# Optimization experiments

Measured on AMD Instinct MI355X. Metric: run time of the kernel, lower is better.

Reference implementation:

```python
import jax, jax.numpy as jnp
import numpy as np

D_MODEL = 1024
D_FF = 4096
NUM_EXPERTS = 8
NUM_SLOTS = 2
LN_EPS = 1e-5


def setup_inputs() -> dict:
    key = jax.random.key(0)
    ks = jax.random.split(key, 4)
    x = jax.random.normal(ks[0], (4, 4096, D_MODEL), dtype=jnp.float32)
    slot_embeds = jax.random.normal(ks[1], (NUM_EXPERTS * NUM_SLOTS, D_MODEL), dtype=jnp.float32) * 0.02
    # per-expert MLP weights, stacked over expert axis (Linear bias=False)
    W1 = jax.random.normal(ks[2], (NUM_EXPERTS, D_MODEL, D_FF), dtype=jnp.float32) * (1.0 / np.sqrt(D_MODEL))
    W2 = jax.random.normal(ks[3], (NUM_EXPERTS, D_FF, D_MODEL), dtype=jnp.float32) * (1.0 / np.sqrt(D_FF))
    ln_gamma = jnp.ones((D_MODEL,), dtype=jnp.float32)
    ln_beta = jnp.zeros((D_MODEL,), dtype=jnp.float32)
    return {"x": x, "slot_embeds": slot_embeds, "W1": W1, "W2": W2,
            "ln_gamma": ln_gamma, "ln_beta": ln_beta}


def reference(x, slot_embeds, W1, W2, ln_gamma, ln_beta):
    B, T, D = x.shape
    E, S = NUM_EXPERTS, NUM_SLOTS
    # logits: [B, T, E*S]
    logits = jnp.einsum('btd,nd->btn', x, slot_embeds) / jnp.sqrt(jnp.asarray(D, x.dtype))
    # dispatch: softmax over tokens (dim=1)
    dispatch = jax.nn.softmax(logits, axis=1)
    slot_in = jnp.einsum('btn,btd->bnd', dispatch, x)  # [B, E*S, D]
    # LayerNorm over last dim
    mu = jnp.mean(slot_in, axis=-1, keepdims=True)
    var = jnp.mean(jnp.square(slot_in - mu), axis=-1, keepdims=True)
    h = (slot_in - mu) * jax.lax.rsqrt(var + LN_EPS) * ln_gamma + ln_beta
    # per-expert MLP as a single batched (grouped) GEMM pair
    h = h.reshape(B, E, S, D)
    u = jax.nn.gelu(jnp.einsum('besd,edf->besf', h, W1), approximate=False)
    slot_out = jnp.einsum('besf,efd->besd', u, W2).reshape(B, E * S, D)
    # combine: softmax over slots (dim=2)
    combine = jax.nn.softmax(logits, axis=2)
    return jnp.einsum('btn,bnd->btd', combine, slot_out)
```

## Files before the change

kernel.cpp:

```cpp
#include <hip/hip_runtime.h>
#include <math.h>

#define NB 4
#define NT 4096
#define ND 1024
#define NS 16
#define NE 8
#define NF 4096

typedef float f32x4 __attribute__((ext_vector_type(4)));

__device__ __forceinline__ float gelu(float v) {
  return 0.5f * v * (1.f + erff(v * 0.70710678118654752f));
}
__device__ __forceinline__ void fma4(float4& a, float s, const float4& v) {
  a.x += s * v.x; a.y += s * v.y; a.z += s * v.z; a.w += s * v.w;
}
__device__ __forceinline__ float4 ld4(const float* p) {
  return *reinterpret_cast<const float4*>(p);
}
__device__ __forceinline__ float4 ld4nt(const float* p) {
  f32x4 v = __builtin_nontemporal_load(reinterpret_cast<const f32x4*>(p));
  return make_float4(v[0], v[1], v[2], v[3]);
}

__global__ __launch_bounds__(256, 4) void k_logits(const float* __restrict__ x,
                                                   const float* __restrict__ se,
                                                   float* __restrict__ logits) {
  const int wave = threadIdx.x >> 6, lane = threadIdx.x & 63;
  const int t0 = blockIdx.x * 16 + wave * 4;
  float acc[64];
#pragma unroll
  for (int j = 0; j < 64; ++j) acc[j] = 0.f;
  for (int it = 0; it < 4; ++it) {
    const int d = it * 256 + lane * 4;
    float4 xv[4];
#pragma unroll
    for (int tt = 0; tt < 4; ++tt)
      xv[tt] = ld4(x + (size_t)(t0 + tt) * ND + d);
#pragma unroll
    for (int n = 0; n < NS; ++n) {
      const float4 sv = ld4(se + (size_t)n * ND + d);
#pragma unroll
      for (int tt = 0; tt < 4; ++tt) {
        acc[tt * 16 + n] += xv[tt].x * sv.x + xv[tt].y * sv.y +
                            xv[tt].z * sv.z + xv[tt].w * sv.w;
      }
    }
  }
#pragma unroll
  for (int k = 0; k < 6; ++k) {
    const int dlt = 1 << k;
    const bool hi = (lane & dlt) != 0;
#pragma unroll
    for (int i = 0; i < (64 >> (k + 1)); ++i) {
      const float a = acc[2 * i], b = acc[2 * i + 1];
      const float send = hi ? a : b;
      const float recv = __shfl_xor(send, dlt, 64);
      acc[i] = (hi ? b : a) + recv;
    }
  }
  logits[(size_t)t0 * NS + lane] = acc[0] * 0.03125f;
}

__global__ __launch_bounds__(256) void k_softmax_stats(const float* __restrict__ logits,
                                                       float* __restrict__ stats) {
  int bn = blockIdx.x;
  int b = bn >> 4, n = bn & 15;
  __shared__ float red[256];
  const float* lp = logits + ((size_t)b * NT) * NS + n;
  float m = -1e30f;
  for (int t = threadIdx.x; t < NT; t += 256) m = fmaxf(m, lp[(size_t)t * NS]);
  red[threadIdx.x] = m; __syncthreads();
  for (int s = 128; s > 0; s >>= 1) {
    if (threadIdx.x < s) red[threadIdx.x] = fmaxf(red[threadIdx.x], red[threadIdx.x + s]);
    __syncthreads();
  }
  m = red[0]; __syncthreads();
  float sm = 0.f;
  for (int t = threadIdx.x; t < NT; t += 256) sm += expf(lp[(size_t)t * NS] - m);
  red[threadIdx.x] = sm; __syncthreads();
  for (int s = 128; s > 0; s >>= 1) {
    if (threadIdx.x < s) red[threadIdx.x] += red[threadIdx.x + s];
    __syncthreads();
  }
  if (threadIdx.x == 0) { stats[bn * 2] = m; stats[bn * 2 + 1] = red[0]; }
}

__global__ __launch_bounds__(256) void k_slot_in(const float* __restrict__ x,
                                                 const float* __restrict__ logits,
                                                 const float* __restrict__ stats,
                                                 float* __restrict__ si_part) {
  __shared__ float s_w[NS][64];
  const int tc = blockIdx.x, b = blockIdx.y;
  const int t0 = tc * 64;
  for (int i = threadIdx.x; i < NS * 64; i += 256) {
    const int n = i >> 6, t = i & 63;
    const float m = stats[(b * NS + n) * 2], s1 = stats[(b * NS + n) * 2 + 1];
    s_w[n][t] = expf(logits[((size_t)b * NT + t0 + t) * NS + n] - m) / s1;
  }
  __syncthreads();
  float4 acc[NS];
#pragma unroll
  for (int n = 0; n < NS; ++n) acc[n] = make_float4(0.f, 0.f, 0.f, 0.f);
  const int d = threadIdx.x * 4;
  const float* xb = x + ((size_t)b * NT + t0) * ND + d;
  float4 xv[2][8];
#pragma unroll
  for (int k = 0; k < 8; ++k) xv[0][k] = ld4(xb + (size_t)k * ND);
#pragma unroll
  for (int g = 0; g < 8; ++g) {
    const int cur = g & 1;
    if (g < 7) {
#pragma unroll
      for (int k = 0; k < 8; ++k)
        xv[cur ^ 1][k] = ld4(xb + (size_t)((g + 1) * 8 + k) * ND);
    }
#pragma unroll
    for (int n = 0; n < NS; ++n) {
      const float4 w0 = ld4(&s_w[n][g * 8]);
      const float4 w1 = ld4(&s_w[n][g * 8 + 4]);
      fma4(acc[n], w0.x, xv[cur][0]); fma4(acc[n], w0.y, xv[cur][1]);
      fma4(acc[n], w0.z, xv[cur][2]); fma4(acc[n], w0.w, xv[cur][3]);
      fma4(acc[n], w1.x, xv[cur][4]); fma4(acc[n], w1.y, xv[cur][5]);
      fma4(acc[n], w1.z, xv[cur][6]); fma4(acc[n], w1.w, xv[cur][7]);
    }
  }
#pragma unroll
  for (int n = 0; n < NS; ++n)
    *reinterpret_cast<float4*>(si_part + (((size_t)tc * 4 + b) * NS + n) * ND + d) = acc[n];
}

__global__ __launch_bounds__(256) void k_reduce_si(const float* __restrict__ si_part,
                                                   float* __restrict__ slot_in) {
  const int i = blockIdx.x * 256 + threadIdx.x;
  const int row = i >> 10, d = i & 1023;
  const int b = row >> 4, n = row & 15;
  float sum = 0.f;
  for (int tc = 0; tc < 64; ++tc)
    sum += si_part[(((size_t)tc * 4 + b) * NS + n) * ND + d];
  slot_in[i] = sum;
}

__global__ __launch_bounds__(256) void k_layernorm(float* __restrict__ slot_in,
                                                   const float* __restrict__ gamma,
                                                   const float* __restrict__ beta) {
  int row = blockIdx.x;
  __shared__ float red[256];
  float* rp = slot_in + (size_t)row * ND;
  float v[4];
  float sum = 0.f;
#pragma unroll
  for (int j = 0; j < 4; ++j) { v[j] = rp[threadIdx.x + j * 256]; sum += v[j]; }
  red[threadIdx.x] = sum; __syncthreads();
  for (int s = 128; s > 0; s >>= 1) {
    if (threadIdx.x < s) red[threadIdx.x] += red[threadIdx.x + s];
    __syncthreads();
  }
  float mu = red[0] * (1.f / ND); __syncthreads();
  float vs = 0.f;
#pragma unroll
  for (int j = 0; j < 4; ++j) { float t = v[j] - mu; vs += t * t; }
  red[threadIdx.x] = vs; __syncthreads();
  for (int s = 128; s > 0; s >>= 1) {
    if (threadIdx.x < s) red[threadIdx.x] += red[threadIdx.x + s];
    __syncthreads();
  }
  float rstd = rsqrtf(red[0] * (1.f / ND) + 1e-5f);
#pragma unroll
  for (int j = 0; j < 4; ++j) {
    int dd = threadIdx.x + j * 256;
    rp[dd] = (v[j] - mu) * rstd * gamma[dd] + beta[dd];
  }
}

__global__ __launch_bounds__(256) void k_mlp1(const float* __restrict__ h,
                                              const float* __restrict__ W1,
                                              float* __restrict__ u_part) {
  __shared__ float s_h[64][8];
  const int ft = blockIdx.x, dc = blockIdx.y, e = blockIdx.z;
  for (int i = threadIdx.x; i < 512; i += 256) {
    const int dd = i >> 3, j = i & 7;
    const int b = j >> 1, s = j & 1;
    s_h[dd][j] = h[((size_t)b * NS + e * 2 + s) * ND + dc * 64 + dd];
  }
  __syncthreads();
  float4 acc[8];
#pragma unroll
  for (int j = 0; j < 8; ++j) acc[j] = make_float4(0.f, 0.f, 0.f, 0.f);
  const int f = ft * 1024 + threadIdx.x * 4;
  const float* wb = W1 + ((size_t)e * ND + dc * 64) * NF + f;
  float4 wv[2][8];
#pragma unroll
  for (int k = 0; k < 8; ++k) wv[0][k] = ld4nt(wb + (size_t)k * NF);
#pragma unroll
  for (int g = 0; g < 8; ++g) {
    const int cur = g & 1;
    if (g < 7) {
#pragma unroll
      for (int k = 0; k < 8; ++k)
        wv[cur ^ 1][k] = ld4nt(wb + (size_t)((g + 1) * 8 + k) * NF);
    }
#pragma unroll
    for (int k = 0; k < 8; ++k) {
      const int dd = g * 8 + k;
      const float4 h0 = ld4(&s_h[dd][0]);
      const float4 h1 = ld4(&s_h[dd][4]);
      fma4(acc[0], h0.x, wv[cur][k]); fma4(acc[1], h0.y, wv[cur][k]);
      fma4(acc[2], h0.z, wv[cur][k]); fma4(acc[3], h0.w, wv[cur][k]);
      fma4(acc[4], h1.x, wv[cur][k]); fma4(acc[5], h1.y, wv[cur][k]);
      fma4(acc[6], h1.z, wv[cur][k]); fma4(acc[7], h1.w, wv[cur][k]);
    }
  }
#pragma unroll
  for (int j = 0; j < 8; ++j) {
    const int b = j >> 1, s = j & 1;
    const size_t row = ((size_t)b * NE + e) * 2 + s;
    *reinterpret_cast<float4*>(u_part + ((size_t)dc * 64 + row) * NF + f) = acc[j];
  }
}

__global__ __launch_bounds__(256) void k_mlp2(const float* __restrict__ u_part,
                                              const float* __restrict__ W2,
                                              float* __restrict__ so_part) {
  __shared__ float s_u[64][8];
  const int fc = blockIdx.x, e = blockIdx.y;
  for (int i = threadIdx.x; i < 512; i += 256) {
    const int j = i >> 6, ff = i & 63;
    const int b = j >> 1, s = j & 1;
    const size_t urow = ((size_t)b * NE + e) * 2 + s;
    float sum = 0.f;
    for (int dcc = 0; dcc < 16; ++dcc)
      sum += u_part[((size_t)dcc * 64 + urow) * NF + fc * 64 + ff];
    s_u[ff][j] = gelu(sum);
  }
  __syncthreads();
  float4 acc[8];
#pragma unroll
  for (int j = 0; j < 8; ++j) acc[j] = make_float4(0.f, 0.f, 0.f, 0.f);
  const int d = threadIdx.x * 4;
  const float* wb = W2 + ((size_t)e * NF + fc * 64) * ND + d;
  float4 wv[2][8];
#pragma unroll
  for (int k = 0; k < 8; ++k) wv[0][k] = ld4nt(wb + (size_t)k * ND);
#pragma unroll
  for (int g = 0; g < 8; ++g) {
    const int cur = g & 1;
    if (g < 7) {
#pragma unroll
      for (int k = 0; k < 8; ++k)
        wv[cur ^ 1][k] = ld4nt(wb + (size_t)((g + 1) * 8 + k) * ND);
    }
#pragma unroll
    for (int k = 0; k < 8; ++k) {
      const int ff = g * 8 + k;
      const float4 u0 = ld4(&s_u[ff][0]);
      const float4 u1 = ld4(&s_u[ff][4]);
      fma4(acc[0], u0.x, wv[cur][k]); fma4(acc[1], u0.y, wv[cur][k]);
      fma4(acc[2], u0.z, wv[cur][k]); fma4(acc[3], u0.w, wv[cur][k]);
      fma4(acc[4], u1.x, wv[cur][k]); fma4(acc[5], u1.y, wv[cur][k]);
      fma4(acc[6], u1.z, wv[cur][k]); fma4(acc[7], u1.w, wv[cur][k]);
    }
  }
#pragma unroll
  for (int j = 0; j < 8; ++j) {
    const int b = j >> 1, s = j & 1;
    const size_t row = (size_t)b * NS + e * 2 + s;
    *reinterpret_cast<float4*>(so_part + ((size_t)fc * 64 + row) * ND + d) = acc[j];
  }
}

__global__ __launch_bounds__(256) void k_reduce_so(const float* __restrict__ so_part,
                                                   float* __restrict__ slot_out) {
  const int i = blockIdx.x * 256 + threadIdx.x;
  float sum = 0.f;
  for (int fc = 0; fc < 64; ++fc)
    sum += so_part[(size_t)fc * 65536 + i];
  slot_out[i] = sum;
}

__global__ __launch_bounds__(256) void k_combine(const float* __restrict__ logits,
                                                 const float* __restrict__ slot_out,
                                                 float* __restrict__ out) {
  __shared__ float s_so[NS * ND];
  const int tb = blockIdx.x, b = blockIdx.y;
  for (int i = threadIdx.x; i < NS * ND; i += 256)
    s_so[i] = slot_out[(size_t)b * NS * ND + i];
  __syncthreads();
  const int wave = threadIdx.x >> 6, lane = threadIdx.x & 63;
  const int tbase = tb * 64 + wave * 16;
  for (int g = 0; g < 4; ++g) {
    const int t0 = tbase + g * 4;
    float c[4][NS];
#pragma unroll
    for (int tt = 0; tt < 4; ++tt) {
      const float* lp = logits + ((size_t)b * NT + t0 + tt) * NS;
      float l[NS];
      float m = -1e30f;
#pragma unroll
      for (int n = 0; n < NS; ++n) { l[n] = lp[n]; m = fmaxf(m, l[n]); }
      float s = 0.f;
#pragma unroll
      for (int n = 0; n < NS; ++n) { l[n] = expf(l[n] - m); s += l[n]; }
      const float rs = 1.f / s;
#pragma unroll
      for (int n = 0; n < NS; ++n) c[tt][n] = l[n] * rs;
    }
#pragma unroll
    for (int it = 0; it < 4; ++it) {
      const int d = it * 256 + lane * 4;
      float4 acc[4];
#pragma unroll
      for (int tt = 0; tt < 4; ++tt) acc[tt] = make_float4(0.f, 0.f, 0.f, 0.f);
#pragma unroll
      for (int n = 0; n < NS; ++n) {
        const float4 sv = ld4(&s_so[n * ND + d]);
        fma4(acc[0], c[0][n], sv); fma4(acc[1], c[1][n], sv);
        fma4(acc[2], c[2][n], sv); fma4(acc[3], c[3][n], sv);
      }
#pragma unroll
      for (int tt = 0; tt < 4; ++tt)
        *reinterpret_cast<float4*>(out + ((size_t)b * NT + t0 + tt) * ND + d) = acc[tt];
    }
  }
}

extern "C" void kernel_launch(void* const* d_in, const int* in_sizes, int n_in,
                              void* d_out, int out_size, void* d_ws, size_t ws_size,
                              hipStream_t stream) {
  const float* x     = (const float*)d_in[0];
  const float* se    = (const float*)d_in[1];
  const float* W1    = (const float*)d_in[2];
  const float* W2    = (const float*)d_in[3];
  const float* gamma = (const float*)d_in[4];
  const float* beta  = (const float*)d_in[5];
  float* out = (float*)d_out;

  float* ws       = (float*)d_ws;
  float* logits   = ws;
  float* stats    = ws + 262144;
  float* slot_in  = ws + 262400;
  float* slot_out = ws + 327936;
  float* si_part  = ws + 393472;
  float* u_part   = ws + 4587776;
  float* so_part  = ws + 8782080;

  k_logits<<<1024, 256, 0, stream>>>(x, se, logits);
  k_softmax_stats<<<NB * NS, 256, 0, stream>>>(logits, stats);
  k_slot_in<<<dim3(64, NB), 256, 0, stream>>>(x, logits, stats, si_part);
  k_reduce_si<<<256, 256, 0, stream>>>(si_part, slot_in);
  k_layernorm<<<NB * NS, 256, 0, stream>>>(slot_in, gamma, beta);
  k_mlp1<<<dim3(4, 16, NE), 256, 0, stream>>>(slot_in, W1, u_part);
  k_mlp2<<<dim3(64, NE), 256, 0, stream>>>(u_part, W2, so_part);
  k_reduce_so<<<256, 256, 0, stream>>>(so_part, slot_out);
  k_combine<<<dim3(64, NB), 256, 0, stream>>>(logits, slot_out, out);
}
```

Before: 448.2 us.

## Stream x and expert weights into LDS via async global_load_lds double buffering

In the slot_in, mlp1 and mlp2 kernels, register-held prefetches of x, W1 and W2 tiles are replaced with direct global-to-LDS loads (`__builtin_amdgcn_global_load_lds`, 16 bytes per lane) into a two-stage shared-memory ring. Each thread then reads its float4 from LDS, and a barrier ends each stage. The aim is to free vector registers and overlap streaming of the large weight and activation tiles with the FMA work. In exchange, each block now reserves 64KB of extra LDS, which lowers occupancy. It also adds a barrier per stage and drops the nontemporal load hint on the weight streams.

Result: slower. 462.5 us (+3.2%).

```diff
diff --git a/kernel.cpp b/kernel.cpp
--- a/kernel.cpp
+++ b/kernel.cpp
@@ -8,8 +8,6 @@
 #define NE 8
 #define NF 4096
 
-typedef float f32x4 __attribute__((ext_vector_type(4)));
-
 __device__ __forceinline__ float gelu(float v) {
   return 0.5f * v * (1.f + erff(v * 0.70710678118654752f));
 }
@@ -19,9 +17,10 @@
 __device__ __forceinline__ float4 ld4(const float* p) {
   return *reinterpret_cast<const float4*>(p);
 }
-__device__ __forceinline__ float4 ld4nt(const float* p) {
-  f32x4 v = __builtin_nontemporal_load(reinterpret_cast<const f32x4*>(p));
-  return make_float4(v[0], v[1], v[2], v[3]);
+__device__ __forceinline__ void gload_lds16(const float* gsrc, float* ldst) {
+  __builtin_amdgcn_global_load_lds(
+      (const __attribute__((address_space(1))) unsigned int*)gsrc,
+      (__attribute__((address_space(3))) unsigned int*)ldst, 16, 0, 0);
 }
 
 __global__ __launch_bounds__(256, 4) void k_logits(const float* __restrict__ x,
@@ -92,8 +91,16 @@
                                                  const float* __restrict__ stats,
                                                  float* __restrict__ si_part) {
   __shared__ float s_w[NS][64];
+  __shared__ float s_x[2][8 * 1024];
   const int tc = blockIdx.x, b = blockIdx.y;
   const int t0 = tc * 64;
+  const int wv = threadIdx.x >> 6, ln = threadIdx.x & 63;
+  const float* xb0 = x + ((size_t)b * NT + t0) * ND;
+#pragma unroll
+  for (int q = 0; q < 8; ++q) {
+    const int c = wv * 8 + q;
+    gload_lds16(xb0 + c * 256 + ln * 4, &s_x[0][c * 256]);
+  }
   for (int i = threadIdx.x; i < NS * 64; i += 256) {
     const int n = i >> 6, t = i & 63;
     const float m = stats[(b * NS + n) * 2], s1 = stats[(b * NS + n) * 2 + 1];
@@ -103,32 +110,33 @@
   float4 acc[NS];
 #pragma unroll
   for (int n = 0; n < NS; ++n) acc[n] = make_float4(0.f, 0.f, 0.f, 0.f);
-  const int d = threadIdx.x * 4;
-  const float* xb = x + ((size_t)b * NT + t0) * ND + d;
-  float4 xv[2][8];
-#pragma unroll
-  for (int k = 0; k < 8; ++k) xv[0][k] = ld4(xb + (size_t)k * ND);
-#pragma unroll
+  const int d4 = threadIdx.x * 4;
   for (int g = 0; g < 8; ++g) {
-    const int cur = g & 1;
     if (g < 7) {
-#pragma unroll
-      for (int k = 0; k < 8; ++k)
-        xv[cur ^ 1][k] = ld4(xb + (size_t)((g + 1) * 8 + k) * ND);
-    }
+      const float* src = xb0 + (size_t)(g + 1) * 8 * ND;
+#pragma unroll
+      for (int q = 0; q < 8; ++q) {
+        const int c = wv * 8 + q;
+        gload_lds16(src + c * 256 + ln * 4, &s_x[(g + 1) & 1][c * 256]);
+      }
+    }
+    const float* xt = &s_x[g & 1][0];
+    float4 xv[8];
+#pragma unroll
+    for (int k = 0; k < 8; ++k) xv[k] = ld4(xt + k * 1024 + d4);
 #pragma unroll
     for (int n = 0; n < NS; ++n) {
-      const float4 w0 = ld4(&s_w[n][g * 8]);
-      const float4 w1 = ld4(&s_w[n][g * 8 + 4]);
-      fma4(acc[n], w0.x, xv[cur][0]); fma4(acc[n], w0.y, xv[cur][1]);
-      fma4(acc[n], w0.z, xv[cur][2]); fma4(acc[n], w0.w, xv[cur][3]);
-      fma4(acc[n], w1.x, xv[cur][4]); fma4(acc[n], w1.y, xv[cur][5]);
-      fma4(acc[n], w1.z, xv[cur][6]); fma4(acc[n], w1.w, xv[cur][7]);
-    }
+      const float* wn = &s_w[n][g * 8];
+      fma4(acc[n], wn[0], xv[0]); fma4(acc[n], wn[1], xv[1]);
+      fma4(acc[n], wn[2], xv[2]); fma4(acc[n], wn[3], xv[3]);
+      fma4(acc[n], wn[4], xv[4]); fma4(acc[n], wn[5], xv[5]);
+      fma4(acc[n], wn[6], xv[6]); fma4(acc[n], wn[7], xv[7]);
+    }
+    __syncthreads();
   }
 #pragma unroll
   for (int n = 0; n < NS; ++n)
-    *reinterpret_cast<float4*>(si_part + (((size_t)tc * 4 + b) * NS + n) * ND + d) = acc[n];
+    *reinterpret_cast<float4*>(si_part + (((size_t)tc * 4 + b) * NS + n) * ND + d4) = acc[n];
 }
 
 __global__ __launch_bounds__(256) void k_reduce_si(const float* __restrict__ si_part,
@@ -178,7 +186,16 @@
                                               const float* __restrict__ W1,
                                               float* __restrict__ u_part) {
   __shared__ float s_h[64][8];
+  __shared__ float s_w1[2][8 * 1024];
   const int ft = blockIdx.x, dc = blockIdx.y, e = blockIdx.z;
+  const int wv = threadIdx.x >> 6, ln = threadIdx.x & 63;
+  const float* wb = W1 + ((size_t)e * ND + dc * 64) * NF + ft * 1024;
+#pragma unroll
+  for (int q = 0; q < 8; ++q) {
+    const int c = wv * 8 + q;
+    gload_lds16(wb + (size_t)(c >> 2) * NF + (c & 3) * 256 + ln * 4,
+                &s_w1[0][c * 1024 / 4]);
+  }
   for (int i = threadIdx.x; i < 512; i += 256) {
     const int dd = i >> 3, j = i & 7;
     const int b = j >> 1, s = j & 1;
@@ -188,30 +205,32 @@
   float4 acc[8];
 #pragma unroll
   for (int j = 0; j < 8; ++j) acc[j] = make_float4(0.f, 0.f, 0.f, 0.f);
-  const int f = ft * 1024 + threadIdx.x * 4;
-  const float* wb = W1 + ((size_t)e * ND + dc * 64) * NF + f;
-  float4 wv[2][8];
-#pragma unroll
-  for (int k = 0; k < 8; ++k) wv[0][k] = ld4nt(wb + (size_t)k * NF);
-#pragma unroll
+  const int f4 = threadIdx.x * 4;
   for (int g = 0; g < 8; ++g) {
-    const int cur = g & 1;
     if (g < 7) {
-#pragma unroll
-      for (int k = 0; k < 8; ++k)
-        wv[cur ^ 1][k] = ld4nt(wb + (size_t)((g + 1) * 8 + k) * NF);
-    }
+      const float* src = wb + (size_t)(g + 1) * 8 * NF;
+#pragma unroll
+      for (int q = 0; q < 8; ++q) {
+        const int c = wv * 8 + q;
+        gload_lds16(src + (size_t)(c >> 2) * NF + (c & 3) * 256 + ln * 4,
+                    &s_w1[(g + 1) & 1][c * 256]);
+      }
+    }
+    const float* wt = &s_w1[g & 1][0];
 #pragma unroll
     for (int k = 0; k < 8; ++k) {
       const int dd = g * 8 + k;
+      const float4 w4 = ld4(wt + k * 1024 + f4);
       const float4 h0 = ld4(&s_h[dd][0]);
       const float4 h1 = ld4(&s_h[dd][4]);
-      fma4(acc[0], h0.x, wv[cur][k]); fma4(acc[1], h0.y, wv[cur][k]);
-      fma4(acc[2], h0.z, wv[cur][k]); fma4(acc[3], h0.w, wv[cur][k]);
-      fma4(acc[4], h1.x, wv[cur][k]); fma4(acc[5], h1.y, wv[cur][k]);
-      fma4(acc[6], h1.z, wv[cur][k]); fma4(acc[7], h1.w, wv[cur][k]);
-    }
-  }
+      fma4(acc[0], h0.x, w4); fma4(acc[1], h0.y, w4);
+      fma4(acc[2], h0.z, w4); fma4(acc[3], h0.w, w4);
+      fma4(acc[4], h1.x, w4); fma4(acc[5], h1.y, w4);
+      fma4(acc[6], h1.z, w4); fma4(acc[7], h1.w, w4);
+    }
+    __syncthreads();
+  }
+  const int f = ft * 1024 + f4;
 #pragma unroll
   for (int j = 0; j < 8; ++j) {
     const int b = j >> 1, s = j & 1;
@@ -224,7 +243,15 @@
                                               const float* __restrict__ W2,
                                               float* __restrict__ so_part) {
   __shared__ float s_u[64][8];
+  __shared__ float s_w2[2][8 * 1024];
   const int fc = blockIdx.x, e = blockIdx.y;
+  const int wv = threadIdx.x >> 6, ln = threadIdx.x & 63;
+  const float* wb = W2 + ((size_t)e * NF + fc * 64) * ND;
+#pragma unroll
+  for (int q = 0; q < 8; ++q) {
+    const int c = wv * 8 + q;
+    gload_lds16(wb + c * 256 + ln * 4, &s_w2[0][c * 256]);
+  }
   for (int i = threadIdx.x; i < 512; i += 256) {
     const int j = i >> 6, ff = i & 63;
     const int b = j >> 1, s = j & 1;
@@ -238,35 +265,35 @@
   float4 acc[8];
 #pragma unroll
   for (int j = 0; j < 8; ++j) acc[j] = make_float4(0.f, 0.f, 0.f, 0.f);
-  const int d = threadIdx.x * 4;
-  const float* wb = W2 + ((size_t)e * NF + fc * 64) * ND + d;
-  float4 wv[2][8];
-#pragma unroll
-  for (int k = 0; k < 8; ++k) wv[0][k] = ld4nt(wb + (size_t)k * ND);
-#pragma unroll
+  const int d4 = threadIdx.x * 4;
   for (int g = 0; g < 8; ++g) {
-    const int cur = g & 1;
     if (g < 7) {
-#pragma unroll
-      for (int k = 0; k < 8; ++k)
-        wv[cur ^ 1][k] = ld4nt(wb + (size_t)((g + 1) * 8 + k) * ND);
-    }
+      const float* src = wb + (size_t)(g + 1) * 8 * ND;
+#pragma unroll
+      for (int q = 0; q < 8; ++q) {
+        const int c = wv * 8 + q;
+        gload_lds16(src + c * 256 + ln * 4, &s_w2[(g + 1) & 1][c * 256]);
+      }
+    }
+    const float* wt = &s_w2[g & 1][0];
 #pragma unroll
     for (int k = 0; k < 8; ++k) {
       const int ff = g * 8 + k;
+      const float4 w4 = ld4(wt + k * 1024 + d4);
       const float4 u0 = ld4(&s_u[ff][0]);
       const float4 u1 = ld4(&s_u[ff][4]);
-      fma4(acc[0], u0.x, wv[cur][k]); fma4(acc[1], u0.y, wv[cur][k]);
-      fma4(acc[2], u0.z, wv[cur][k]); fma4(acc[3], u0.w, wv[cur][k]);
-      fma4(acc[4], u1.x, wv[cur][k]); fma4(acc[5], u1.y, wv[cur][k]);
-      fma4(acc[6], u1.z, wv[cur][k]); fma4(acc[7], u1.w, wv[cur][k]);
-    }
+      fma4(acc[0], u0.x, w4); fma4(acc[1], u0.y, w4);
+      fma4(acc[2], u0.z, w4); fma4(acc[3], u0.w, w4);
+      fma4(acc[4], u1.x, w4); fma4(acc[5], u1.y, w4);
+      fma4(acc[6], u1.z, w4); fma4(acc[7], u1.w, w4);
+    }
+    __syncthreads();
   }
 #pragma unroll
   for (int j = 0; j < 8; ++j) {
     const int b = j >> 1, s = j & 1;
     const size_t row = (size_t)b * NS + e * 2 + s;
-    *reinterpret_cast<float4*>(so_part + ((size_t)fc * 64 + row) * ND + d) = acc[j];
+    *reinterpret_cast<float4*>(so_part + ((size_t)fc * 64 + row) * ND + d4) = acc[j];
   }
 }
 
```
